# Kernel tuning notes

Hardware: AMD Instinct MI355X
Metric: run time of the kernel (lower is better)

Reference implementation:

```python
import jax, jax.numpy as jnp
import numpy as np


def setup_inputs() -> dict:
    key = jax.random.key(0)
    k1, k2 = jax.random.split(key)
    B, C, H, W = 8, 128, 128, 128
    Ho, Wo = 128, 128
    src = jax.random.normal(k1, (B, C, H, W), dtype=jnp.float32)
    # normalized grid coords in [-1, 1], last dim = (x, y)
    norm_grid = jax.random.uniform(k2, (B, Ho, Wo, 2), dtype=jnp.float32) * 2.0 - 1.0
    return {"src": src, "norm_grid": norm_grid}


def _bilinear_sample_one(img, gx, gy):
    # img: [C, H, W]; gx, gy: [Ho, Wo] normalized coords in [-1, 1]
    C, H, W = img.shape
    # align_corners=True unnormalization
    x = (gx + 1.0) * 0.5 * (W - 1)
    y = (gy + 1.0) * 0.5 * (H - 1)

    x0 = jnp.floor(x)
    y0 = jnp.floor(y)
    x1 = x0 + 1.0
    y1 = y0 + 1.0

    wx1 = x - x0  # weight toward x1
    wy1 = y - y0  # weight toward y1
    wx0 = 1.0 - wx1
    wy0 = 1.0 - wy1

    x0i = x0.astype(jnp.int32)
    x1i = x1.astype(jnp.int32)
    y0i = y0.astype(jnp.int32)
    y1i = y1.astype(jnp.int32)

    def in_bounds(yi, xi):
        return ((yi >= 0) & (yi <= H - 1) & (xi >= 0) & (xi <= W - 1)).astype(img.dtype)

    def gather(yi, xi, mask):
        yc = jnp.clip(yi, 0, H - 1)
        xc = jnp.clip(xi, 0, W - 1)
        # [C, Ho, Wo]; zeros padding via mask
        return img[:, yc, xc] * mask[None, :, :]

    v00 = gather(y0i, x0i, in_bounds(y0i, x0i))
    v01 = gather(y0i, x1i, in_bounds(y0i, x1i))
    v10 = gather(y1i, x0i, in_bounds(y1i, x0i))
    v11 = gather(y1i, x1i, in_bounds(y1i, x1i))

    out = (v00 * (wy0 * wx0)[None]
           + v01 * (wy0 * wx1)[None]
           + v10 * (wy1 * wx0)[None]
           + v11 * (wy1 * wx1)[None])
    return out  # [C, Ho, Wo]


def reference(src, norm_grid):
    # src: [B, C, H, W]; norm_grid: [B, Ho, Wo, 2] with (x, y) in [-1, 1]
    src32 = src.astype(jnp.float32)
    gx = norm_grid[..., 0].astype(jnp.float32)
    gy = norm_grid[..., 1].astype(jnp.float32)
    return jax.vmap(_bilinear_sample_one)(src32, gx, gy)  # [B, C, Ho, Wo]
```

## Files before the change

### kernel.cpp

```cpp
#include <hip/hip_runtime.h>


constexpr int PLANE_ELEMS = 128 * 128;

typedef const __attribute__((address_space(1))) char gchar_t;
typedef __attribute__((address_space(3))) char lchar_t;

__device__ __forceinline__ float bsample(const float* plane, float gx, float gy) {
    const float x = fmaf(gx, 63.5f, 63.5f);
    const float y = fmaf(gy, 63.5f, 63.5f);
    const float xf = fminf(floorf(x), 126.0f);
    const float yf = fminf(floorf(y), 126.0f);
    const float wx = x - xf;
    const float wy = y - yf;
    const int idx = (int)fmaf(yf, 128.0f, xf);
    const float v00 = plane[idx];
    const float v01 = plane[idx + 1];
    const float v10 = plane[idx + 128];
    const float v11 = plane[idx + 129];
    const float v0 = fmaf(wx, v01 - v00, v00);
    const float v1 = fmaf(wx, v11 - v10, v10);
    return fmaf(wy, v1 - v0, v0);
}

__global__ __launch_bounds__(512, 4)
void FunctionAffineGridBilinearSample_54039278519070_kernel(
        const float* __restrict__ src,
        const float* __restrict__ grid,
        float* __restrict__ out)
{
    __shared__ float plane[PLANE_ELEMS];

    const int bid = blockIdx.x;
    const int b   = bid >> 7;
    const int tid = threadIdx.x;

    const char* gsrc = (const char*)(src + ((size_t)bid << 14));
    char* lbase = (char*)plane;
    #pragma unroll
    for (int it = 0; it < 8; ++it) {
        const int byteoff = (it * 512 + tid) * 16;
        __builtin_amdgcn_global_load_lds(
            (gchar_t*)(gsrc + byteoff),
            (lchar_t*)(lbase + byteoff),
            16, 0, 0);
    }
    __syncthreads();

    const float* ggrid = grid + ((size_t)b << 15);
    float* gout = out + ((size_t)bid << 14);

    #pragma unroll
    for (int it = 0; it < 8; ++it) {
        const int p0 = (it * 512 + tid) * 4;
        const float4 g01 = *(const float4*)(ggrid + 2 * p0);
        const float4 g23 = *(const float4*)(ggrid + 2 * p0 + 4);

        float4 r;
        r.x = bsample(plane, g01.x, g01.y);
        r.y = bsample(plane, g01.z, g01.w);
        r.z = bsample(plane, g23.x, g23.y);
        r.w = bsample(plane, g23.z, g23.w);

        *(float4*)(gout + p0) = r;
    }
}

extern "C" void kernel_launch(void* const* d_in, const int* in_sizes, int n_in,
                              void* d_out, int out_size, void* d_ws, size_t ws_size,
                              hipStream_t stream) {
    const float* src  = (const float*)d_in[0];
    const float* grid = (const float*)d_in[1];
    float* out = (float*)d_out;

    FunctionAffineGridBilinearSample_54039278519070_kernel<<<1024, 512, 0, stream>>>(
        src, grid, out);
}
```

Baseline: 118.3 us.

## Process four channel planes per block with double-buffered LDS and reused grid coords

Each block now handles four consecutive channel planes of one batch with 1024 threads. It computes the bilinear indices and weights once, keeps them in registers, and reuses them across all four channels. The next plane is prefetched into a second 64KB LDS buffer with global_load_lds while the current plane is sampled. The aim is to cut redundant grid loads and coordinate math and to hide the source-plane load latency. In exchange each block needs 128KB of dynamic LDS, which allows at most one block per CU, and the launch drops to 256 blocks, so occupancy falls and register pressure rises.

```diff
diff --git a/kernel.cpp b/kernel.cpp
--- a/kernel.cpp
+++ b/kernel.cpp
@@ -1,68 +1,99 @@
 #include <hip/hip_runtime.h>
 
 
-constexpr int PLANE_ELEMS = 128 * 128;
+constexpr int PLANE        = 128 * 128;
+constexpr int PLANE_BYTES  = PLANE * 4;
+constexpr int TPB          = 1024;
+constexpr int PPB          = 4;
 
 typedef const __attribute__((address_space(1))) char gchar_t;
 typedef __attribute__((address_space(3))) char lchar_t;
 
-__device__ __forceinline__ float bsample(const float* plane, float gx, float gy) {
+__device__ __forceinline__ void coord(float gx, float gy,
+                                      int& idx, float& wx, float& wy) {
     const float x = fmaf(gx, 63.5f, 63.5f);
     const float y = fmaf(gy, 63.5f, 63.5f);
     const float xf = fminf(floorf(x), 126.0f);
     const float yf = fminf(floorf(y), 126.0f);
-    const float wx = x - xf;
-    const float wy = y - yf;
-    const int idx = (int)fmaf(yf, 128.0f, xf);
-    const float v00 = plane[idx];
-    const float v01 = plane[idx + 1];
-    const float v10 = plane[idx + 128];
-    const float v11 = plane[idx + 129];
+    wx = x - xf;
+    wy = y - yf;
+    idx = (int)fmaf(yf, 128.0f, xf);
+}
+
+__device__ __forceinline__ float lerp2(const float* __restrict__ buf,
+                                       int idx, float wx, float wy) {
+    const float v00 = buf[idx];
+    const float v01 = buf[idx + 1];
+    const float v10 = buf[idx + 128];
+    const float v11 = buf[idx + 129];
     const float v0 = fmaf(wx, v01 - v00, v00);
     const float v1 = fmaf(wx, v11 - v10, v10);
     return fmaf(wy, v1 - v0, v0);
 }
 
-__global__ __launch_bounds__(512, 4)
+__global__ __launch_bounds__(TPB, 4)
 void FunctionAffineGridBilinearSample_54039278519070_kernel(
         const float* __restrict__ src,
         const float* __restrict__ grid,
         float* __restrict__ out)
 {
-    __shared__ float plane[PLANE_ELEMS];
+    extern __shared__ float lds[];
+    const int tid  = threadIdx.x;
+    const int pid0 = blockIdx.x * PPB;
+    const int b    = pid0 >> 7;
 
-    const int bid = blockIdx.x;
-    const int b   = bid >> 7;
-    const int tid = threadIdx.x;
+    {
+        const char* gs = (const char*)(src + (size_t)pid0 * PLANE);
+        char* lb = (char*)lds;
+        #pragma unroll
+        for (int it = 0; it < 4; ++it) {
+            const int off = (it * TPB + tid) * 16;
+            __builtin_amdgcn_global_load_lds(
+                (gchar_t*)(gs + off), (lchar_t*)(lb + off), 16, 0, 0);
+        }
+    }
 
-    const char* gsrc = (const char*)(src + ((size_t)bid << 14));
-    char* lbase = (char*)plane;
+    const float* g2 = grid + ((size_t)b << 15);
+    int   idx[16];
+    float wx[16], wy[16];
     #pragma unroll
-    for (int it = 0; it < 8; ++it) {
-        const int byteoff = (it * 512 + tid) * 16;
-        __builtin_amdgcn_global_load_lds(
-            (gchar_t*)(gsrc + byteoff),
-            (lchar_t*)(lbase + byteoff),
-            16, 0, 0);
+    for (int i4 = 0; i4 < 4; ++i4) {
+        const int p0 = (i4 * TPB + tid) * 4;
+        const float4 a = *(const float4*)(g2 + 2 * p0);
+        const float4 c = *(const float4*)(g2 + 2 * p0 + 4);
+        coord(a.x, a.y, idx[i4*4+0], wx[i4*4+0], wy[i4*4+0]);
+        coord(a.z, a.w, idx[i4*4+1], wx[i4*4+1], wy[i4*4+1]);
+        coord(c.x, c.y, idx[i4*4+2], wx[i4*4+2], wy[i4*4+2]);
+        coord(c.z, c.w, idx[i4*4+3], wx[i4*4+3], wy[i4*4+3]);
     }
     __syncthreads();
 
-    const float* ggrid = grid + ((size_t)b << 15);
-    float* gout = out + ((size_t)bid << 14);
+    #pragma unroll
+    for (int ch = 0; ch < PPB; ++ch) {
+        if (ch < PPB - 1) {
+            const char* gs = (const char*)(src + (size_t)(pid0 + ch + 1) * PLANE);
+            char* lb = (char*)lds + ((ch + 1) & 1) * PLANE_BYTES;
+            #pragma unroll
+            for (int it = 0; it < 4; ++it) {
+                const int off = (it * TPB + tid) * 16;
+                __builtin_amdgcn_global_load_lds(
+                    (gchar_t*)(gs + off), (lchar_t*)(lb + off), 16, 0, 0);
+            }
+        }
 
-    #pragma unroll
-    for (int it = 0; it < 8; ++it) {
-        const int p0 = (it * 512 + tid) * 4;
-        const float4 g01 = *(const float4*)(ggrid + 2 * p0);
-        const float4 g23 = *(const float4*)(ggrid + 2 * p0 + 4);
-
-        float4 r;
-        r.x = bsample(plane, g01.x, g01.y);
-        r.y = bsample(plane, g01.z, g01.w);
-        r.z = bsample(plane, g23.x, g23.y);
-        r.w = bsample(plane, g23.z, g23.w);
-
-        *(float4*)(gout + p0) = r;
+        const float* buf  = lds + (ch & 1) * PLANE;
+        float*       gout = out + (size_t)(pid0 + ch) * PLANE;
+        #pragma unroll
+        for (int i4 = 0; i4 < 4; ++i4) {
+            const int p0 = (i4 * TPB + tid) * 4;
+            float4 r;
+            r.x = lerp2(buf, idx[i4*4+0], wx[i4*4+0], wy[i4*4+0]);
+            r.y = lerp2(buf, idx[i4*4+1], wx[i4*4+1], wy[i4*4+1]);
+            r.z = lerp2(buf, idx[i4*4+2], wx[i4*4+2], wy[i4*4+2]);
+            r.w = lerp2(buf, idx[i4*4+3], wx[i4*4+3], wy[i4*4+3]);
+            *(float4*)(gout + p0) = r;
+        }
+        __syncthreads();
     }
 }
 
@@ -73,6 +104,10 @@
     const float* grid = (const float*)d_in[1];
     float* out = (float*)d_out;
 
-    FunctionAffineGridBilinearSample_54039278519070_kernel<<<1024, 512, 0, stream>>>(
-        src, grid, out);
+    hipFuncSetAttribute(
+        (const void*)FunctionAffineGridBilinearSample_54039278519070_kernel,
+        hipFuncAttributeMaxDynamicSharedMemorySize, 2 * PLANE_BYTES);
+
+    FunctionAffineGridBilinearSample_54039278519070_kernel
+        <<<256, TPB, 2 * PLANE_BYTES, stream>>>(src, grid, out);
 }
```

Result: no change. 119.2 us (+0.7%).
